# Kernel optimization log

Measured on AMD Instinct MI355X. Metric: run time of the kernel, lower is better.

Reference implementation:

```python
import jax, jax.numpy as jnp
import numpy as np

B, L, HID = 1, 2048, 4096
H, KV, D = 32, 2, 128
ROT = int(D * 0.5)  # partial rotary dims per head
THETA = 10000.0
SCALE = D ** -0.5


def _rope_tables(L, rot, theta):
    inv_freq = 1.0 / (theta ** (np.arange(0, rot, 2, dtype=np.float32) / rot))  # [rot/2]
    t = np.arange(L, dtype=np.float32)
    freqs = np.outer(t, inv_freq)  # [L, rot/2]
    return jnp.asarray(np.cos(freqs)), jnp.asarray(np.sin(freqs))


def setup_inputs() -> dict:
    key = jax.random.key(0)
    ks = jax.random.split(key, 8)
    s = HID ** -0.5
    x = jax.random.normal(ks[0], (B, L, HID), dtype=jnp.float32)
    Wq = jax.random.normal(ks[1], (HID, H * D), dtype=jnp.float32) * s
    Wk = jax.random.normal(ks[2], (HID, KV * D), dtype=jnp.float32) * s
    Wv = jax.random.normal(ks[3], (HID, KV * D), dtype=jnp.float32) * s
    Wo = jax.random.normal(ks[4], (H * D, HID), dtype=jnp.float32) * s
    bq = jax.random.normal(ks[5], (H * D,), dtype=jnp.float32) * 0.01
    bk = jax.random.normal(ks[6], (KV * D,), dtype=jnp.float32) * 0.01
    bv = jax.random.normal(ks[7], (KV * D,), dtype=jnp.float32) * 0.01
    cos, sin = _rope_tables(L, ROT, THETA)
    # additive causal mask
    causal = jnp.tril(jnp.ones((L, L), dtype=bool))
    attention_mask = jnp.where(causal, 0.0, -1e9)[None, None].astype(jnp.float32)
    return {"x": x, "Wq": Wq, "bq": bq, "Wk": Wk, "bk": bk, "Wv": Wv, "bv": bv,
            "Wo": Wo, "cos": cos, "sin": sin, "attention_mask": attention_mask}


def _apply_rope(t, cos, sin):
    # t: [B, h, L, D]; rotary on first ROT dims, pass-through on the rest
    t_rot, t_pass = t[..., :ROT], t[..., ROT:]
    x1, x2 = t_rot[..., : ROT // 2], t_rot[..., ROT // 2:]
    c = cos[None, None]  # [1,1,L,ROT/2]
    s = sin[None, None]
    rot = jnp.concatenate([x1 * c - x2 * s, x2 * c + x1 * s], axis=-1)
    return jnp.concatenate([rot, t_pass], axis=-1)


def reference(x, Wq, bq, Wk, bk, Wv, bv, Wo, cos, sin, attention_mask):
    Bx, Lx, _ = x.shape
    q = (x @ Wq + bq).reshape(Bx, Lx, H, D).transpose(0, 2, 1, 3)   # [B,H,L,D]
    k = (x @ Wk + bk).reshape(Bx, Lx, KV, D).transpose(0, 2, 1, 3)  # [B,KV,L,D]
    v = (x @ Wv + bv).reshape(Bx, Lx, KV, D).transpose(0, 2, 1, 3)
    q = _apply_rope(q, cos, sin)
    k = _apply_rope(k, cos, sin)
    # GQA: repeat KV heads
    rep = H // KV
    k = jnp.repeat(k, rep, axis=1)  # [B,H,L,D]
    v = jnp.repeat(v, rep, axis=1)
    w = jnp.einsum('bhqd,bhkd->bhqk', q, k) * SCALE + attention_mask
    w = jax.nn.softmax(w, axis=-1)
    o = jnp.einsum('bhqk,bhkd->bhqd', w, v)
    o = o.transpose(0, 2, 1, 3).reshape(Bx, Lx, H * D)
    return o @ Wo
```

## Files before the change

kernel.cpp:

```cpp
#include <hip/hip_runtime.h>
#include <stdint.h>

#define L_SEQ 2048
#define HID   4096
#define NH    32
#define NKV   2
#define DH    128
#define NQKV  4608
#define QSCALE 0.088388347648318447f

typedef __bf16 bf16x8 __attribute__((ext_vector_type(8)));
typedef float  f32x4  __attribute__((ext_vector_type(4)));

__device__ __forceinline__ unsigned short f2bf(float f) {
  union { float f; unsigned u; } cv; cv.f = f;
  unsigned u = cv.u;
  return (unsigned short)((u + 0x7fffu + ((u >> 16) & 1u)) >> 16);
}
__device__ __forceinline__ float bf2f(unsigned short h) {
  union { unsigned u; float f; } cv; cv.u = (unsigned)h << 16; return cv.f;
}

#define GLL16(gsrc, ldst)                                                              \
  __builtin_amdgcn_global_load_lds(                                                    \
      (const __attribute__((address_space(1))) unsigned int*)(gsrc),                   \
      (__attribute__((address_space(3))) unsigned int*)(ldst), 16, 0, 0)

__global__ __launch_bounds__(256) void cast_bf16_kernel(const float* __restrict__ in,
                                                        unsigned short* __restrict__ out,
                                                        int n4) {
  int i = blockIdx.x * 256 + threadIdx.x;
  if (i >= n4) return;
  float4 v = reinterpret_cast<const float4*>(in)[i];
  ushort4 o;
  o.x = f2bf(v.x); o.y = f2bf(v.y); o.z = f2bf(v.z); o.w = f2bf(v.w);
  reinterpret_cast<ushort4*>(out)[i] = o;
}

__global__ __launch_bounds__(256) void transpose_cast_kernel(const float* __restrict__ in,
                                                             unsigned short* __restrict__ out,
                                                             int R, int C) {
  __shared__ float tile[64][65];
  const int c0 = blockIdx.x * 64, r0 = blockIdx.y * 64;
  const int tid = threadIdx.x;
  #pragma unroll
  for (int it = 0; it < 4; ++it) {
    int row = it * 16 + (tid >> 4);
    float4 v = *reinterpret_cast<const float4*>(&in[(size_t)(r0 + row) * C + c0 + (tid & 15) * 4]);
    tile[row][(tid & 15) * 4 + 0] = v.x;
    tile[row][(tid & 15) * 4 + 1] = v.y;
    tile[row][(tid & 15) * 4 + 2] = v.z;
    tile[row][(tid & 15) * 4 + 3] = v.w;
  }
  __syncthreads();
  #pragma unroll
  for (int it = 0; it < 8; ++it) {
    int c  = it * 8 + (tid >> 5);
    int rp = tid & 31;
    unsigned u = (unsigned)f2bf(tile[2 * rp][c]) | ((unsigned)f2bf(tile[2 * rp + 1][c]) << 16);
    *reinterpret_cast<unsigned*>(&out[(size_t)(c0 + c) * R + r0 + 2 * rp]) = u;
  }
}

#define TBM 128
#define TBN 128
#define TBK 64

template <int OUT_BF16>
__global__ __launch_bounds__(256, 2) void gemm128_kernel(const unsigned short* __restrict__ A,
                                                         const unsigned short* __restrict__ Bt,
                                                         void* __restrict__ Cv,
                                                         int M, int N, int K) {
  __shared__ __attribute__((aligned(16))) unsigned short As[2][TBM * TBK];
  __shared__ __attribute__((aligned(16))) unsigned short Bs[2][TBN * TBK];
  const int tid = threadIdx.x;
  const int wave = tid >> 6, lane = tid & 63;
  const int lg = lane >> 4, ll = lane & 15;
  const int wm = wave >> 1, wn = wave & 1;

  int gx = gridDim.x, nwg = gx * gridDim.y;
  int flat = blockIdx.y * gx + blockIdx.x;
  int bx = blockIdx.x, by = blockIdx.y;
  if ((nwg & 7) == 0) {
    int t = (flat & 7) * (nwg >> 3) + (flat >> 3);
    bx = t % gx; by = t / gx;
  }
  const int m0 = by * TBM, n0 = bx * TBN;

  f32x4 acc[4][4] = {};
  const int NT = K >> 6;

  auto stage = [&](int t, int buf) {
    const int k0 = t * TBK;
    #pragma unroll
    for (int i = 0; i < 4; ++i) {
      int ci  = (i * 4 + wave) * 64 + lane;
      int row = ci >> 3;
      int cg  = (ci & 7) ^ (row & 7);
      GLL16(A + (size_t)(m0 + row) * K + k0 + cg * 8, &As[buf][(i * 4 + wave) * 512]);
    }
    #pragma unroll
    for (int i = 0; i < 4; ++i) {
      int ci  = (i * 4 + wave) * 64 + lane;
      int row = ci >> 3;
      int cg  = (ci & 7) ^ (row & 7);
      GLL16(Bt + (size_t)(n0 + row) * K + k0 + cg * 8, &Bs[buf][(i * 4 + wave) * 512]);
    }
  };

  stage(0, 0);
  stage(1, 1);

  for (int t = 0; t < NT; ++t) {
    const int cur = t & 1;
    if (t + 1 < NT) asm volatile("s_waitcnt vmcnt(8)" ::: "memory");
    else            asm volatile("s_waitcnt vmcnt(0)" ::: "memory");
    __builtin_amdgcn_s_barrier();

    const unsigned short* Ac = &As[cur][0];
    const unsigned short* Bc = &Bs[cur][0];
    bf16x8 afr[2][4], bfr[2][4];
    #pragma unroll
    for (int kk = 0; kk < 2; ++kk)
      #pragma unroll
      for (int i = 0; i < 4; ++i) {
        int ra = wm * 64 + i * 16 + ll;
        afr[kk][i] = *reinterpret_cast<const bf16x8*>(
            &Ac[ra * 64 + (((kk * 4 + lg) ^ (ra & 7)) * 8)]);
        int rb = wn * 64 + i * 16 + ll;
        bfr[kk][i] = *reinterpret_cast<const bf16x8*>(
            &Bc[rb * 64 + (((kk * 4 + lg) ^ (rb & 7)) * 8)]);
      }
    __builtin_amdgcn_s_setprio(1);
    #pragma unroll
    for (int kk = 0; kk < 2; ++kk)
      #pragma unroll
      for (int i = 0; i < 4; ++i)
        #pragma unroll
        for (int j = 0; j < 4; ++j)
          acc[i][j] = __builtin_amdgcn_mfma_f32_16x16x32_bf16(afr[kk][i], bfr[kk][j],
                                                              acc[i][j], 0, 0, 0);
    __builtin_amdgcn_s_setprio(0);

    __builtin_amdgcn_s_barrier();
    if (t + 2 < NT) stage(t + 2, cur);
  }

  #pragma unroll
  for (int i = 0; i < 4; ++i)
    #pragma unroll
    for (int j = 0; j < 4; ++j) {
      int col  = n0 + wn * 64 + j * 16 + ll;
      int rowb = m0 + wm * 64 + i * 16 + lg * 4;
      #pragma unroll
      for (int r = 0; r < 4; ++r) {
        size_t idx = (size_t)(rowb + r) * N + col;
        if (OUT_BF16) ((unsigned short*)Cv)[idx] = f2bf(acc[i][j][r]);
        else          ((float*)Cv)[idx]          = acc[i][j][r];
      }
    }
}

__global__ __launch_bounds__(128) void qkv_post_kernel(const unsigned short* __restrict__ qkv,
                                                       const float* __restrict__ bq,
                                                       const float* __restrict__ bk,
                                                       const float* __restrict__ bv,
                                                       const float* __restrict__ cosT,
                                                       const float* __restrict__ sinT,
                                                       unsigned short* __restrict__ qb,
                                                       unsigned short* __restrict__ kb,
                                                       unsigned short* __restrict__ vt) {
  int l = blockIdx.x, y = blockIdx.y, d = threadIdx.x;
  if (y < 34) {
    const bool isq = (y < 32);
    const int hh = isq ? y : (y - 32);
    const float* bias = isq ? bq : bk;
    size_t base = (size_t)l * NQKV + (isq ? 0 : 4096) + hh * DH;
    float v = bf2f(qkv[base + d]) + bias[hh * DH + d];
    float o;
    if (d < 32) {
      float x2 = bf2f(qkv[base + d + 32]) + bias[hh * DH + d + 32];
      o = v * cosT[l * 32 + d] - x2 * sinT[l * 32 + d];
    } else if (d < 64) {
      int i = d - 32;
      float x1 = bf2f(qkv[base + i]) + bias[hh * DH + i];
      o = v * cosT[l * 32 + i] + x1 * sinT[l * 32 + i];
    } else {
      o = v;
    }
    if (isq) qb[((size_t)hh * L_SEQ + l) * DH + d] = f2bf(o * QSCALE);
    else     kb[((size_t)hh * L_SEQ + l) * DH + d] = f2bf(o);
  } else {
    int g = y - 34;
    float o = bf2f(qkv[(size_t)l * NQKV + 4352 + g * DH + d]) + bv[g * DH + d];
    vt[((size_t)g * DH + d) * L_SEQ + l] = f2bf(o);
  }
}

__global__ __launch_bounds__(256) void attn_kernel(const unsigned short* __restrict__ qg,
                                                   const unsigned short* __restrict__ kb,
                                                   const unsigned short* __restrict__ vt,
                                                   unsigned short* __restrict__ ob) {
  __shared__ __attribute__((aligned(16))) unsigned short Ks[2][64 * 128];
  __shared__ __attribute__((aligned(16))) unsigned short Vs[2][128 * 64];
  __shared__ __attribute__((aligned(16))) unsigned short Ps[4][16 * 64];

  const int pair = blockIdx.x, h = blockIdx.y;
  const int g = h >> 4;
  const int tid = threadIdx.x, wave = tid >> 6, lane = tid & 63;
  const int lg = lane >> 4, ll = lane & 15;

  const int krow = (lane >> 4);
  const int kcg0 = (lane & 15);
  const int vrow = (lane >> 3);
  const int vcg0 = (lane & 7);

  #pragma unroll
  for (int seg = 0; seg < 2; ++seg) {
    const int qt = seg ? (31 - pair) : pair;
    const int q0 = qt * 64 + wave * 16;

    bf16x8 qf[4];
    #pragma unroll
    for (int f = 0; f < 4; ++f)
      qf[f] = *reinterpret_cast<const bf16x8*>(
          qg + ((size_t)h * L_SEQ + q0 + ll) * DH + f * 32 + lg * 8);

    f32x4 of[8] = {};
    float m = -1e30f, lsum = 0.f;

    const int kvN = qt + 1;
    int cur = 0;

    #pragma unroll
    for (int c = 0; c < 4; ++c) {
      int issue = wave * 4 + c;
      int rk = issue * 4 + krow;
      GLL16(kb + ((size_t)g * L_SEQ + rk) * DH + (kcg0 ^ (rk & 7)) * 8, &Ks[0][issue * 512]);
      int rv = issue * 8 + vrow;
      GLL16(vt + ((size_t)g * DH + rv) * L_SEQ + (vcg0 ^ (rv & 7)) * 8, &Vs[0][issue * 512]);
    }
    __syncthreads();

    for (int t = 0; t < kvN; ++t) {
      if (t + 1 < kvN) {
        int kv1 = (t + 1) * 64;
        #pragma unroll
        for (int c = 0; c < 4; ++c) {
          int issue = wave * 4 + c;
          int rk = issue * 4 + krow;
          GLL16(kb + ((size_t)g * L_SEQ + kv1 + rk) * DH + (kcg0 ^ (rk & 7)) * 8,
                &Ks[cur ^ 1][issue * 512]);
          int rv = issue * 8 + vrow;
          GLL16(vt + ((size_t)g * DH + rv) * L_SEQ + kv1 + (vcg0 ^ (rv & 7)) * 8,
                &Vs[cur ^ 1][issue * 512]);
        }
      }

      f32x4 s[4] = {};
      const unsigned short* Kc = &Ks[cur][0];
      #pragma unroll
      for (int cf = 0; cf < 4; ++cf) {
        bf16x8 kf[4];
        #pragma unroll
        for (int f = 0; f < 4; ++f) {
          int rk = cf * 16 + ll;
          int cc = (f * 4 + lg) ^ (rk & 7);
          kf[f] = *reinterpret_cast<const bf16x8*>(&Kc[rk * 128 + cc * 8]);
        }
        __builtin_amdgcn_s_setprio(1);
        #pragma unroll
        for (int f = 0; f < 4; ++f)
          s[cf] = __builtin_amdgcn_mfma_f32_16x16x32_bf16(kf[f], qf[f], s[cf], 0, 0, 0);
        __builtin_amdgcn_s_setprio(0);
      }

      if (t == qt) {
        #pragma unroll
        for (int cf = 0; cf < 4; ++cf)
          #pragma unroll
          for (int r = 0; r < 4; ++r)
            if (cf * 16 + lg * 4 + r > wave * 16 + ll) s[cf][r] = -1e30f;
      }

      float pmax = -1e30f;
      #pragma unroll
      for (int cf = 0; cf < 4; ++cf)
        #pragma unroll
        for (int r = 0; r < 4; ++r) pmax = fmaxf(pmax, s[cf][r]);
      if (!__all(pmax - m <= 8.f)) {
        float mx = fmaxf(pmax, __shfl_xor(pmax, 16));
        mx = fmaxf(mx, __shfl_xor(mx, 32));
        float mnew = fmaxf(m, mx);
        float alpha = __expf(m - mnew);
        m = mnew;
        lsum *= alpha;
        float af[4];
        #pragma unroll
        for (int r = 0; r < 4; ++r) af[r] = __shfl(alpha, lg * 4 + r);
        #pragma unroll
        for (int ds = 0; ds < 8; ++ds)
          #pragma unroll
          for (int r = 0; r < 4; ++r) of[ds][r] *= af[r];
      }

      unsigned short* pw = &Ps[wave][0];
      float psum = 0.f;
      #pragma unroll
      for (int cf = 0; cf < 4; ++cf) {
        float p0 = __expf(s[cf][0] - m), p1 = __expf(s[cf][1] - m);
        float p2 = __expf(s[cf][2] - m), p3 = __expf(s[cf][3] - m);
        psum += (p0 + p1) + (p2 + p3);
        uint2 w;
        w.x = (unsigned)f2bf(p0) | ((unsigned)f2bf(p1) << 16);
        w.y = (unsigned)f2bf(p2) | ((unsigned)f2bf(p3) << 16);
        int chunk = (cf * 2 + (lg >> 1)) ^ (ll & 7);
        *reinterpret_cast<uint2*>(&pw[ll * 64 + chunk * 8 + (lg & 1) * 4]) = w;
      }
      lsum += psum;

      bf16x8 pa[2];
      #pragma unroll
      for (int ks = 0; ks < 2; ++ks)
        pa[ks] = *reinterpret_cast<const bf16x8*>(
            &pw[ll * 64 + (((ks * 4 + lg) ^ (ll & 7)) * 8)]);

      const unsigned short* Vc = &Vs[cur][0];
      #pragma unroll
      for (int ds = 0; ds < 8; ++ds) {
        bf16x8 vf[2];
        #pragma unroll
        for (int ks = 0; ks < 2; ++ks) {
          int dl = ds * 16 + ll;
          int cc = (ks * 4 + lg) ^ (dl & 7);
          vf[ks] = *reinterpret_cast<const bf16x8*>(&Vc[dl * 64 + cc * 8]);
        }
        __builtin_amdgcn_s_setprio(1);
        #pragma unroll
        for (int ks = 0; ks < 2; ++ks)
          of[ds] = __builtin_amdgcn_mfma_f32_16x16x32_bf16(pa[ks], vf[ks], of[ds], 0, 0, 0);
        __builtin_amdgcn_s_setprio(0);
      }

      __syncthreads();
      cur ^= 1;
    }

    float tot = lsum + __shfl_xor(lsum, 16);
    tot += __shfl_xor(tot, 32);
    float inv = 1.f / tot;
    float invr[4];
    #pragma unroll
    for (int r = 0; r < 4; ++r) invr[r] = __shfl(inv, lg * 4 + r);
    #pragma unroll
    for (int ds = 0; ds < 8; ++ds)
      #pragma unroll
      for (int r = 0; r < 4; ++r) {
        int row = q0 + lg * 4 + r;
        ob[(size_t)row * (NH * DH) + h * DH + ds * 16 + ll] = f2bf(of[ds][r] * invr[r]);
      }
    __syncthreads();
  }
}

extern "C" void kernel_launch(void* const* d_in, const int* in_sizes, int n_in,
                              void* d_out, int out_size, void* d_ws, size_t ws_size,
                              hipStream_t stream) {
  (void)in_sizes; (void)n_in; (void)out_size; (void)ws_size;
  const float* x    = (const float*)d_in[0];
  const float* Wq   = (const float*)d_in[1];
  const float* bq   = (const float*)d_in[2];
  const float* Wk   = (const float*)d_in[3];
  const float* bk   = (const float*)d_in[4];
  const float* Wv   = (const float*)d_in[5];
  const float* bv   = (const float*)d_in[6];
  const float* Wo   = (const float*)d_in[7];
  const float* cosT = (const float*)d_in[8];
  const float* sinT = (const float*)d_in[9];

  char* ws = (char*)d_ws;
  size_t off = 0;
  auto alloc = [&](size_t bytes) { void* p = ws + off; off += (bytes + 255) & ~(size_t)255; return p; };
  unsigned short* xb     = (unsigned short*)alloc((size_t)L_SEQ * HID * 2);
  unsigned short* Wqkvt  = (unsigned short*)alloc((size_t)NQKV * HID * 2);
  unsigned short* Wot    = (unsigned short*)alloc((size_t)HID * HID * 2);
  unsigned short* qkvlin = (unsigned short*)alloc((size_t)L_SEQ * NQKV * 2);
  unsigned short* qbuf   = (unsigned short*)alloc((size_t)NH * L_SEQ * DH * 2);
  unsigned short* kbuf   = (unsigned short*)alloc((size_t)NKV * L_SEQ * DH * 2);
  unsigned short* vtb    = (unsigned short*)alloc((size_t)NKV * DH * L_SEQ * 2);
  unsigned short* attno  = (unsigned short*)alloc((size_t)L_SEQ * HID * 2);

  cast_bf16_kernel<<<(L_SEQ * HID / 4 + 255) / 256, 256, 0, stream>>>(x, xb, L_SEQ * HID / 4);
  transpose_cast_kernel<<<dim3(HID / 64, HID / 64), 256, 0, stream>>>(Wq, Wqkvt, HID, HID);
  transpose_cast_kernel<<<dim3(256 / 64, HID / 64), 256, 0, stream>>>(Wk, Wqkvt + (size_t)4096 * HID, HID, 256);
  transpose_cast_kernel<<<dim3(256 / 64, HID / 64), 256, 0, stream>>>(Wv, Wqkvt + (size_t)4352 * HID, HID, 256);
  transpose_cast_kernel<<<dim3(HID / 64, HID / 64), 256, 0, stream>>>(Wo, Wot, HID, HID);

  gemm128_kernel<1><<<dim3(NQKV / TBN, L_SEQ / TBM), 256, 0, stream>>>(xb, Wqkvt, qkvlin, L_SEQ, NQKV, HID);

  qkv_post_kernel<<<dim3(L_SEQ, 36), 128, 0, stream>>>(qkvlin, bq, bk, bv, cosT, sinT,
                                                       qbuf, kbuf, vtb);

  attn_kernel<<<dim3(16, NH), 256, 0, stream>>>(qbuf, kbuf, vtb, attno);

  gemm128_kernel<0><<<dim3(HID / TBN, L_SEQ / TBM), 256, 0, stream>>>(attno, Wot, (float*)d_out, L_SEQ, HID, HID);
}
```

Baseline: 352.7 us.

## Fuse bias, RoPE and head-layout scatter into QKV GEMM epilogue; reorder staging barrier

Result: faster. 310.6 us (-12.0%).

```diff
diff --git a/kernel.cpp b/kernel.cpp
--- a/kernel.cpp
+++ b/kernel.cpp
@@ -62,14 +62,45 @@
   }
 }
 
+__global__ __launch_bounds__(256) void vtrans_kernel(const unsigned short* __restrict__ in,
+                                                     unsigned short* __restrict__ out) {
+  __shared__ unsigned short tile[64][72];
+  const int l0 = blockIdx.x * 64, d0 = blockIdx.y * 64, g = blockIdx.z;
+  const int tid = threadIdx.x;
+  #pragma unroll
+  for (int it = 0; it < 2; ++it) {
+    int l = it * 32 + (tid >> 3);
+    *reinterpret_cast<uint4*>(&tile[l][(tid & 7) * 8]) =
+        *reinterpret_cast<const uint4*>(&in[((size_t)g * L_SEQ + l0 + l) * DH + d0 + (tid & 7) * 8]);
+  }
+  __syncthreads();
+  #pragma unroll
+  for (int it = 0; it < 2; ++it) {
+    int d = it * 32 + (tid >> 3);
+    unsigned short tmp[8];
+    #pragma unroll
+    for (int e = 0; e < 8; ++e) tmp[e] = tile[(tid & 7) * 8 + e][d];
+    *reinterpret_cast<uint4*>(&out[((size_t)g * DH + d0 + d) * L_SEQ + l0 + (tid & 7) * 8]) =
+        *reinterpret_cast<uint4*>(tmp);
+  }
+}
+
 #define TBM 128
 #define TBN 128
 #define TBK 64
 
-template <int OUT_BF16>
+template <int MODE>
 __global__ __launch_bounds__(256, 2) void gemm128_kernel(const unsigned short* __restrict__ A,
                                                          const unsigned short* __restrict__ Bt,
-                                                         void* __restrict__ Cv,
+                                                         float* __restrict__ C,
+                                                         const float* __restrict__ bq,
+                                                         const float* __restrict__ bk,
+                                                         const float* __restrict__ bv,
+                                                         const float* __restrict__ cosT,
+                                                         const float* __restrict__ sinT,
+                                                         unsigned short* __restrict__ qb,
+                                                         unsigned short* __restrict__ kb,
+                                                         unsigned short* __restrict__ vlin,
                                                          int M, int N, int K) {
   __shared__ __attribute__((aligned(16))) unsigned short As[2][TBM * TBK];
   __shared__ __attribute__((aligned(16))) unsigned short Bs[2][TBN * TBK];
@@ -131,6 +162,10 @@
         bfr[kk][i] = *reinterpret_cast<const bf16x8*>(
             &Bc[rb * 64 + (((kk * 4 + lg) ^ (rb & 7)) * 8)]);
       }
+    asm volatile("s_waitcnt lgkmcnt(0)" ::: "memory");
+    __builtin_amdgcn_s_barrier();
+    if (t + 2 < NT) stage(t + 2, cur);
+
     __builtin_amdgcn_s_setprio(1);
     #pragma unroll
     for (int kk = 0; kk < 2; ++kk)
@@ -141,59 +176,60 @@
           acc[i][j] = __builtin_amdgcn_mfma_f32_16x16x32_bf16(afr[kk][i], bfr[kk][j],
                                                               acc[i][j], 0, 0, 0);
     __builtin_amdgcn_s_setprio(0);
-
-    __builtin_amdgcn_s_barrier();
-    if (t + 2 < NT) stage(t + 2, cur);
-  }
-
-  #pragma unroll
-  for (int i = 0; i < 4; ++i)
+  }
+
+  if (MODE == 0) {
+    #pragma unroll
+    for (int i = 0; i < 4; ++i)
+      #pragma unroll
+      for (int j = 0; j < 4; ++j) {
+        int col  = n0 + wn * 64 + j * 16 + ll;
+        int rowb = m0 + wm * 64 + i * 16 + lg * 4;
+        #pragma unroll
+        for (int r = 0; r < 4; ++r)
+          C[(size_t)(rowb + r) * N + col] = acc[i][j][r];
+      }
+  } else {
+    const int region = (n0 < 4096) ? 0 : ((n0 < 4352) ? 1 : 2);
+    const int hh = (region == 0) ? (n0 >> 7) : ((region == 1) ? ((n0 - 4096) >> 7) : ((n0 - 4352) >> 7));
+    const float* bias = (region == 0) ? bq : ((region == 1) ? bk : bv);
     #pragma unroll
     for (int j = 0; j < 4; ++j) {
-      int col  = n0 + wn * 64 + j * 16 + ll;
-      int rowb = m0 + wm * 64 + i * 16 + lg * 4;
-      #pragma unroll
-      for (int r = 0; r < 4; ++r) {
-        size_t idx = (size_t)(rowb + r) * N + col;
-        if (OUT_BF16) ((unsigned short*)Cv)[idx] = f2bf(acc[i][j][r]);
-        else          ((float*)Cv)[idx]          = acc[i][j][r];
-      }
-    }
-}
-
-__global__ __launch_bounds__(128) void qkv_post_kernel(const unsigned short* __restrict__ qkv,
-                                                       const float* __restrict__ bq,
-                                                       const float* __restrict__ bk,
-                                                       const float* __restrict__ bv,
-                                                       const float* __restrict__ cosT,
-                                                       const float* __restrict__ sinT,
-                                                       unsigned short* __restrict__ qb,
-                                                       unsigned short* __restrict__ kb,
-                                                       unsigned short* __restrict__ vt) {
-  int l = blockIdx.x, y = blockIdx.y, d = threadIdx.x;
-  if (y < 34) {
-    const bool isq = (y < 32);
-    const int hh = isq ? y : (y - 32);
-    const float* bias = isq ? bq : bk;
-    size_t base = (size_t)l * NQKV + (isq ? 0 : 4096) + hh * DH;
-    float v = bf2f(qkv[base + d]) + bias[hh * DH + d];
-    float o;
-    if (d < 32) {
-      float x2 = bf2f(qkv[base + d + 32]) + bias[hh * DH + d + 32];
-      o = v * cosT[l * 32 + d] - x2 * sinT[l * 32 + d];
-    } else if (d < 64) {
-      int i = d - 32;
-      float x1 = bf2f(qkv[base + i]) + bias[hh * DH + i];
-      o = v * cosT[l * 32 + i] + x1 * sinT[l * 32 + i];
-    } else {
-      o = v;
-    }
-    if (isq) qb[((size_t)hh * L_SEQ + l) * DH + d] = f2bf(o * QSCALE);
-    else     kb[((size_t)hh * L_SEQ + l) * DH + d] = f2bf(o);
-  } else {
-    int g = y - 34;
-    float o = bf2f(qkv[(size_t)l * NQKV + 4352 + g * DH + d]) + bv[g * DH + d];
-    vt[((size_t)g * DH + d) * L_SEQ + l] = f2bf(o);
+      float bj = bias[hh * DH + wn * 64 + j * 16 + ll];
+      #pragma unroll
+      for (int i = 0; i < 4; ++i)
+        #pragma unroll
+        for (int r = 0; r < 4; ++r) acc[i][j][r] += bj;
+    }
+    if (region < 2 && wn == 0) {
+      #pragma unroll
+      for (int i = 0; i < 4; ++i)
+        #pragma unroll
+        for (int r = 0; r < 4; ++r) {
+          int l = m0 + wm * 64 + i * 16 + lg * 4 + r;
+          float c0 = cosT[l * 32 + ll],      s0 = sinT[l * 32 + ll];
+          float c1 = cosT[l * 32 + 16 + ll], s1 = sinT[l * 32 + 16 + ll];
+          float x10 = acc[i][0][r], x20 = acc[i][2][r];
+          float x11 = acc[i][1][r], x21 = acc[i][3][r];
+          acc[i][0][r] = x10 * c0 - x20 * s0;
+          acc[i][2][r] = x20 * c0 + x10 * s0;
+          acc[i][1][r] = x11 * c1 - x21 * s1;
+          acc[i][3][r] = x21 * c1 + x11 * s1;
+        }
+    }
+    const float scale = (region == 0) ? QSCALE : 1.f;
+    unsigned short* dst = (region == 0) ? qb : ((region == 1) ? kb : vlin);
+    #pragma unroll
+    for (int i = 0; i < 4; ++i)
+      #pragma unroll
+      for (int j = 0; j < 4; ++j) {
+        int d = wn * 64 + j * 16 + ll;
+        #pragma unroll
+        for (int r = 0; r < 4; ++r) {
+          int l = m0 + wm * 64 + i * 16 + lg * 4 + r;
+          dst[((size_t)hh * L_SEQ + l) * DH + d] = f2bf(acc[i][j][r] * scale);
+        }
+      }
   }
 }
 
@@ -381,14 +417,14 @@
   char* ws = (char*)d_ws;
   size_t off = 0;
   auto alloc = [&](size_t bytes) { void* p = ws + off; off += (bytes + 255) & ~(size_t)255; return p; };
-  unsigned short* xb     = (unsigned short*)alloc((size_t)L_SEQ * HID * 2);
-  unsigned short* Wqkvt  = (unsigned short*)alloc((size_t)NQKV * HID * 2);
-  unsigned short* Wot    = (unsigned short*)alloc((size_t)HID * HID * 2);
-  unsigned short* qkvlin = (unsigned short*)alloc((size_t)L_SEQ * NQKV * 2);
-  unsigned short* qbuf   = (unsigned short*)alloc((size_t)NH * L_SEQ * DH * 2);
-  unsigned short* kbuf   = (unsigned short*)alloc((size_t)NKV * L_SEQ * DH * 2);
-  unsigned short* vtb    = (unsigned short*)alloc((size_t)NKV * DH * L_SEQ * 2);
-  unsigned short* attno  = (unsigned short*)alloc((size_t)L_SEQ * HID * 2);
+  unsigned short* xb    = (unsigned short*)alloc((size_t)L_SEQ * HID * 2);
+  unsigned short* Wqkvt = (unsigned short*)alloc((size_t)NQKV * HID * 2);
+  unsigned short* Wot   = (unsigned short*)alloc((size_t)HID * HID * 2);
+  unsigned short* qbuf  = (unsigned short*)alloc((size_t)NH * L_SEQ * DH * 2);
+  unsigned short* kbuf  = (unsigned short*)alloc((size_t)NKV * L_SEQ * DH * 2);
+  unsigned short* vlin  = (unsigned short*)alloc((size_t)NKV * L_SEQ * DH * 2);
+  unsigned short* vtb   = (unsigned short*)alloc((size_t)NKV * DH * L_SEQ * 2);
+  unsigned short* attno = (unsigned short*)alloc((size_t)L_SEQ * HID * 2);
 
   cast_bf16_kernel<<<(L_SEQ * HID / 4 + 255) / 256, 256, 0, stream>>>(x, xb, L_SEQ * HID / 4);
   transpose_cast_kernel<<<dim3(HID / 64, HID / 64), 256, 0, stream>>>(Wq, Wqkvt, HID, HID);
@@ -396,12 +432,14 @@
   transpose_cast_kernel<<<dim3(256 / 64, HID / 64), 256, 0, stream>>>(Wv, Wqkvt + (size_t)4352 * HID, HID, 256);
   transpose_cast_kernel<<<dim3(HID / 64, HID / 64), 256, 0, stream>>>(Wo, Wot, HID, HID);
 
-  gemm128_kernel<1><<<dim3(NQKV / TBN, L_SEQ / TBM), 256, 0, stream>>>(xb, Wqkvt, qkvlin, L_SEQ, NQKV, HID);
-
-  qkv_post_kernel<<<dim3(L_SEQ, 36), 128, 0, stream>>>(qkvlin, bq, bk, bv, cosT, sinT,
-                                                       qbuf, kbuf, vtb);
+  gemm128_kernel<1><<<dim3(NQKV / TBN, L_SEQ / TBM), 256, 0, stream>>>(
+      xb, Wqkvt, nullptr, bq, bk, bv, cosT, sinT, qbuf, kbuf, vlin, L_SEQ, NQKV, HID);
+
+  vtrans_kernel<<<dim3(L_SEQ / 64, DH / 64, NKV), 256, 0, stream>>>(vlin, vtb);
 
   attn_kernel<<<dim3(16, NH), 256, 0, stream>>>(qbuf, kbuf, vtb, attno);
 
-  gemm128_kernel<0><<<dim3(HID / TBN, L_SEQ / TBM), 256, 0, stream>>>(attno, Wot, (float*)d_out, L_SEQ, HID, HID);
-}
+  gemm128_kernel<0><<<dim3(HID / TBN, L_SEQ / TBM), 256, 0, stream>>>(
+      attno, Wot, (float*)d_out, nullptr, nullptr, nullptr, nullptr, nullptr,
+      nullptr, nullptr, nullptr, L_SEQ, HID, HID);
+}
```
